# Optimization experiments

Measured on AMD Instinct MI355X. Metric: run time of the kernel, lower is better.

The kernel has to match this reference:

```python
import jax, jax.numpy as jnp
import numpy as np
from jax import lax

EQN = 10  # equations per pixel in FlowLayer


def build_a(h, w):
    """Dense constraint basis a[num, EQN, 4*num] (<=2 nonzeros per row), as in FlowLayer.__init__."""
    num = h * w
    a = np.zeros((num, EQN, 4 * num), np.float32)
    for i in range(num):
        right = (i + 1) % w != 0 and i + 1 < num
        down = i + w < num
        if right:
            a[i, 0, 2 * num + i] = 1.0; a[i, 0, i + 1] = -1.0
            a[i, 2, 2 * num + i] = 1.0; a[i, 2, 2 * num + i + 1] = -1.0
            a[i, 4, i] = 1.0;           a[i, 4, i + 1] = -1.0
            a[i, 6, 3 * num + i] = 1.0; a[i, 6, 3 * num + i + 1] = -1.0
            a[i, 8, num + i] = 1.0;     a[i, 8, num + i + 1] = -1.0
        if down:
            a[i, 1, 3 * num + i] = 1.0; a[i, 1, num + i + w] = -1.0
            a[i, 3, 3 * num + i] = 1.0; a[i, 3, 3 * num + i + w] = -1.0
            a[i, 5, num + i] = 1.0;     a[i, 5, num + i + w] = -1.0
            a[i, 7, 2 * num + i] = 1.0; a[i, 7, 2 * num + i + w] = -1.0
            a[i, 9, i] = 1.0;           a[i, 9, i + w] = -1.0
    last = num - 1  # anchor equations for the last pixel
    a[last, 0, 2 * num + last] = 1.0
    a[last, 1, 3 * num + last] = 1.0
    a[last, 2, 2 * num + last] = 1.0
    a[last, 3, 3 * num + last] = 1.0
    a[last, 4, last] = 1.0
    a[last, 5, num + last] = 1.0
    a[last, 6, 3 * num + last] = 1.0
    a[last, 7, 2 * num + last] = 1.0
    a[last, 8, num + last] = 1.0
    a[last, 9, last] = 1.0
    return a


def conv2d(x, w, b):
    y = lax.conv_general_dilated(x, w, (1, 1), 'SAME',
                                 dimension_numbers=('NCHW', 'OIHW', 'NCHW'))
    return y + b[None, :, None, None]


def setup_inputs() -> dict:
    key = jax.random.key(0)
    N, C, H, W, GR = 4, 64, 16, 16, 4
    ks = jax.random.split(key, 12)
    s3, s1 = 0.04, 0.1  # ~1/sqrt(fan_in) scales
    inp = {
        'x': jax.random.normal(ks[0], (N, C, H, W), jnp.float32),
        'grad_w1': jax.random.normal(ks[1], (C, C, 3, 3), jnp.float32) * s3,
        'grad_b1': jnp.zeros((C,), jnp.float32),
        'grad_w2': jax.random.normal(ks[2], (EQN * GR, C, 3, 3), jnp.float32) * s3,
        'grad_b2': jnp.zeros((EQN * GR,), jnp.float32),
        'att_w1': jax.random.normal(ks[3], (C, C, 3, 3), jnp.float32) * s3,
        'att_b1': jnp.zeros((C,), jnp.float32),
        'att_w2': jax.random.normal(ks[4], (EQN * GR, C, 3, 3), jnp.float32) * s3,
        'att_b2': jnp.zeros((EQN * GR,), jnp.float32),
        'se_w1': jax.random.normal(ks[5], (C // 2, C, 1, 1), jnp.float32) * s1,
        'se_b1': jnp.zeros((C // 2,), jnp.float32),
        'se_w2': jax.random.normal(ks[6], (4 * GR, C // 2, 1, 1), jnp.float32) * s1,
        'se_b2': jnp.zeros((4 * GR,), jnp.float32),
        'gn_w': jnp.ones((4 * GR,), jnp.float32),
        'gn_b': jnp.zeros((4 * GR,), jnp.float32),
        'post_w': jax.random.normal(ks[7], (128, 4 * GR, 3, 3), jnp.float32) * s1,
        'post_b': jnp.zeros((128,), jnp.float32),
    }
    return inp


def reference(x, grad_w1, grad_b1, grad_w2, grad_b2,
              att_w1, att_b1, att_w2, att_b2,
              se_w1, se_b1, se_w2, se_b2,
              gn_w, gn_b, post_w, post_b):
    n, c, h, w = x.shape
    gr = gn_w.shape[0] // 4
    num = h * w
    lrelu = lambda t: jax.nn.leaky_relu(t, 0.01)

    grad = conv2d(lrelu(conv2d(x, grad_w1, grad_b1)), grad_w2, grad_b2)      # [n, eqn*gr, h, w]
    att = jax.nn.sigmoid(conv2d(lrelu(conv2d(x, att_w1, att_b1)), att_w2, att_b2))
    pooled = x.mean((2, 3), keepdims=True)                                     # AdaptiveAvgPool2d(1)
    se = jax.nn.sigmoid(conv2d(lrelu(conv2d(pooled, se_w1, se_b1)), se_w2, se_b2))  # [n, 4*gr, 1, 1]

    # reshape(n*gr, EQN, hw).permute -> [B, hw, EQN] -> flatten rows as (pixel, eqn)
    att_f = att.reshape(n * gr, EQN, num).transpose(0, 2, 1).reshape(n * gr, num * EQN)
    grad_f = grad.reshape(n * gr, EQN, num).transpose(0, 2, 1).reshape(n * gr, num * EQN)

    a_flat = jnp.asarray(build_a(h, w)).reshape(num * EQN, 4 * num)  # constant basis
    A = att_f[:, :, None] * a_flat[None]                 # [B, num*EQN, 4*num]
    b_vec = att_f * grad_f                               # [B, num*EQN]
    ATA = jnp.einsum('brj,brk->bjk', A, A)               # [B, 4num, 4num]
    ATB = jnp.einsum('brj,br->bj', A, b_vec)[..., None]  # [B, 4num, 1]
    jitter = jnp.eye(4 * num, dtype=x.dtype) * 1e-12
    sol = jnp.linalg.solve(ATA + jitter[None], ATB)      # [B, 4num, 1]

    y = sol.reshape(n, 4 * gr, h, w)
    # GroupNorm(1, 4*gr): normalize over (C,H,W) per sample
    mu = y.mean((1, 2, 3), keepdims=True)
    var = ((y - mu) ** 2).mean((1, 2, 3), keepdims=True)
    y = (y - mu) / jnp.sqrt(var + 1e-5)
    y = y * gn_w[None, :, None, None] + gn_b[None, :, None, None]
    y = se * y
    return conv2d(y, post_w, post_b)  # [n, 128, h, w]
```

## Files before the change

kernel.cpp:

```cpp
#include <hip/hip_runtime.h>

#define NCHEB 8

typedef __attribute__((ext_vector_type(8))) short vs8;
typedef __attribute__((ext_vector_type(4))) float vf4;
typedef __attribute__((ext_vector_type(16))) float vf16;

__device__ __forceinline__ unsigned short f2bf(float f) {
  union { float f; unsigned int u; } x; x.f = f;
  unsigned int r = (x.u + 0x7FFFu + ((x.u >> 16) & 1u)) >> 16;
  return (unsigned short)r;
}

template<int COUT, int TILES, bool SE>
__global__ __launch_bounds__(256) void k_conv(
    const float* __restrict__ inA, const float* __restrict__ inB,
    const float* __restrict__ wA, const float* __restrict__ bA,
    const float* __restrict__ wB, const float* __restrict__ bB,
    float* __restrict__ outA, float* __restrict__ outB,
    int actA, int actB,
    const float* __restrict__ x,
    const float* __restrict__ sw1, const float* __restrict__ sb1,
    const float* __restrict__ sw2, const float* __restrict__ sb2,
    float* __restrict__ seo) {
  __shared__ unsigned short Xl[256 * 64];
  __shared__ unsigned short Wl[9 * 16 * 64];
  __shared__ float sp[64];
  __shared__ float sh1[32];
  const int b = blockIdx.x;
  const int t = threadIdx.x;

  if (SE && b >= 8 * TILES) {
    const int n = b - 8 * TILES;
    const int c = t >> 2, part = t & 3;
    const float* xp = x + (n * 64 + c) * 256 + part * 64;
    float s = 0.f;
    for (int k = 0; k < 64; ++k) s += xp[k];
    s += __shfl_xor(s, 1, 64);
    s += __shfl_xor(s, 2, 64);
    if (part == 0) sp[c] = s * (1.f / 256.f);
    __syncthreads();
    if (t < 32) {
      float a = sb1[t];
      for (int k = 0; k < 64; ++k) a += sw1[t * 64 + k] * sp[k];
      sh1[t] = a > 0.f ? a : 0.01f * a;
    }
    __syncthreads();
    if (t < 16) {
      float a = sb2[t];
      for (int k = 0; k < 32; ++k) a += sw2[t * 32 + k] * sh1[k];
      seo[n * 16 + t] = 1.f / (1.f + __expf(-a));
    }
    return;
  }

  const int n = b & 3;
  const int q = b >> 2;
  const int br = (q >= TILES) ? 1 : 0;
  const int ct = q - br * TILES;
  const int co0 = ct * 16;
  const float* inp = (br ? inB : inA) + n * 64 * 256;
  const float* wsrc = br ? wB : wA;
  const float* bias = br ? bB : bA;
  float* outp = (br ? outB : outA) + n * COUT * 256;
  const int act = br ? actB : actA;

  {
    const int p = t;
    #pragma unroll
    for (int q8 = 0; q8 < 8; ++q8) {
      vs8 v;
      #pragma unroll
      for (int j = 0; j < 8; ++j) v[j] = (short)f2bf(inp[(8 * q8 + j) * 256 + p]);
      *(vs8*)&Xl[p * 64 + ((q8 ^ (p & 7)) << 3)] = v;
    }
  }
  {
    const int col = t >> 4;
    const int sub = t & 15;
    const int co = co0 + col;
    if (co < COUT) {
      const float* wp = wsrc + (co * 64 + sub * 4) * 9;
      #pragma unroll
      for (int cc = 0; cc < 4; ++cc) {
        const int ci = sub * 4 + cc;
        #pragma unroll
        for (int e = 0; e < 9; ++e)
          Wl[(e * 16 + col) * 64 + (ci ^ ((col & 7) << 3))] = f2bf(wp[cc * 9 + e]);
      }
    } else {
      #pragma unroll
      for (int cc = 0; cc < 4; ++cc) {
        const int ci = sub * 4 + cc;
        #pragma unroll
        for (int e = 0; e < 9; ++e)
          Wl[(e * 16 + col) * 64 + (ci ^ ((col & 7) << 3))] = 0;
      }
    }
  }
  __syncthreads();

  const int w = t >> 6, lane = t & 63;
  const int px = lane & 15, kg = lane >> 4;
  vf4 acc[4];
  #pragma unroll
  for (int mt = 0; mt < 4; ++mt) acc[mt] = (vf4)0.f;

  for (int e = 0; e < 9; ++e) {
    const int dy = e / 3 - 1, dx = e % 3 - 1;
    const bool xok = (dx == 0) || (dx < 0 ? (px > 0) : (px < 15));
    const int xoff = xok ? dx : 0;
    #pragma unroll
    for (int ks = 0; ks < 2; ++ks) {
      vs8 bf = *(const vs8*)&Wl[(e * 16 + px) * 64 + (((ks * 4 + kg) ^ (px & 7)) << 3)];
      #pragma unroll
      for (int mt = 0; mt < 4; ++mt) {
        const int yy = 4 * w + mt + dy;
        if (yy < 0 || yy > 15) continue;
        const int ps = yy * 16 + px + xoff;
        vs8 a = *(const vs8*)&Xl[ps * 64 + (((ks * 4 + kg) ^ (ps & 7)) << 3)];
        if (!xok) a = (vs8)(short)0;
        acc[mt] = __builtin_amdgcn_mfma_f32_16x16x32_bf16(a, bf, acc[mt], 0, 0, 0);
      }
    }
  }

  const int co = co0 + px;
  if (co < COUT) {
    const float bv = bias[co];
    #pragma unroll
    for (int mt = 0; mt < 4; ++mt) {
      const int y = 4 * w + mt;
      vf4 v = acc[mt];
      #pragma unroll
      for (int j = 0; j < 4; ++j) {
        float s = v[j] + bv;
        if (act == 1) s = s > 0.f ? s : 0.01f * s;
        else if (act == 2) s = 1.f / (1.f + __expf(-s));
        v[j] = s;
      }
      *(vf4*)&outp[co * 256 + y * 16 + kg * 4] = v;
    }
  }
}

__global__ __launch_bounds__(512) void k_post(
    const float* __restrict__ sol, const float* __restrict__ se,
    const float* __restrict__ gn_w, const float* __restrict__ gn_b,
    const float* __restrict__ pw, const float* __restrict__ pb,
    float* __restrict__ out) {
  __shared__ unsigned short Hl[256 * 24];
  __shared__ unsigned short Wp[9 * 128 * 24];
  __shared__ float rs[8];
  __shared__ float rs2[8];
  const int n = blockIdx.x;
  const int t = threadIdx.x;
  const int w = t >> 6, lane = t & 63;

  float v[8];
  {
    const vf4* s4 = (const vf4*)(sol + n * 4096 + 8 * t);
    vf4 a = s4[0], b = s4[1];
    v[0]=a[0];v[1]=a[1];v[2]=a[2];v[3]=a[3];v[4]=b[0];v[5]=b[1];v[6]=b[2];v[7]=b[3];
  }
  float s = 0.f, s2 = 0.f;
  #pragma unroll
  for (int k = 0; k < 8; ++k) { s += v[k]; s2 += v[k] * v[k]; }
  #pragma unroll
  for (int o = 1; o <= 32; o <<= 1) { s += __shfl_xor(s, o, 64); s2 += __shfl_xor(s2, o, 64); }
  if (lane == 0) { rs[w] = s; rs2[w] = s2; }

  {
    const int co = t >> 2, sub = t & 3;
    const float* wp0 = pw + (co * 16 + sub * 4) * 9;
    #pragma unroll
    for (int cc = 0; cc < 4; ++cc) {
      const int ci = sub * 4 + cc;
      #pragma unroll
      for (int e = 0; e < 9; ++e)
        Wp[(e * 128 + co) * 24 + ci] = f2bf(wp0[cc * 9 + e]);
    }
  }
  __syncthreads();
  float sm = 0.f, sq = 0.f;
  #pragma unroll
  for (int k = 0; k < 8; ++k) { sm += rs[k]; sq += rs2[k]; }
  const float mu = sm * (1.f / 4096.f);
  const float rstd = rsqrtf(sq * (1.f / 4096.f) - mu * mu + 1e-5f);

  const int c = t >> 5;
  const int p0 = (8 * t) & 255;
  const float sev = se[n * 16 + c];
  const float sc = rstd * gn_w[c] * sev;
  const float of = (gn_b[c] - mu * rstd * gn_w[c]) * sev;
  #pragma unroll
  for (int k = 0; k < 8; ++k) Hl[(p0 + k) * 24 + c] = f2bf(v[k] * sc + of);
  __syncthreads();

  const int cl = lane & 31, h = lane >> 5;
  const int px = cl & 15, y0 = 2 * w + (cl >> 4);
  vf16 acc[4];
  #pragma unroll
  for (int nt = 0; nt < 4; ++nt) acc[nt] = (vf16)0.f;
  for (int e = 0; e < 9; ++e) {
    const int dy = e / 3 - 1, dx = e % 3 - 1;
    const int yy = y0 + dy, xx = px + dx;
    const bool ok = (yy >= 0 && yy < 16 && xx >= 0 && xx < 16);
    const int ps = ok ? yy * 16 + xx : 0;
    vs8 a = *(const vs8*)&Hl[ps * 24 + h * 8];
    if (!ok) a = (vs8)(short)0;
    #pragma unroll
    for (int nt = 0; nt < 4; ++nt) {
      vs8 bf = *(const vs8*)&Wp[(e * 128 + nt * 32 + cl) * 24 + h * 8];
      acc[nt] = __builtin_amdgcn_mfma_f32_32x32x16_bf16(a, bf, acc[nt], 0, 0, 0);
    }
  }
  float* op = out + n * 32768;
  #pragma unroll
  for (int nt = 0; nt < 4; ++nt) {
    const int co = nt * 32 + cl;
    const float bv = pb[co];
    #pragma unroll
    for (int rq = 0; rq < 4; ++rq) {
      vf4 vv;
      #pragma unroll
      for (int j = 0; j < 4; ++j) vv[j] = acc[nt][rq * 4 + j] + bv;
      *(vf4*)&op[co * 256 + 32 * w + 8 * rq + 4 * h] = vv;
    }
  }
}

__global__ __launch_bounds__(64) void k_pcg(
    const float* __restrict__ att, const float* __restrict__ grad,
    float* __restrict__ sol, int maxit, float tol2) {
  const int sys = blockIdx.x >> 1;
  const int wv = blockIdx.x & 1;
  const int l = threadIdx.x;
  const int row = l >> 2, c4 = l & 3;
  const int i0 = 4 * l;

  const int n = sys >> 2, g = sys & 3;
  const float* ab = att + (n * 40 + g * 10) * 256;
  const float* gb = grad + (n * 40 + g * 10) * 256;

  int era, eda, erb, edb, ec, fa, fb;
  if (wv == 0) { fa = 0; fb = 2; era = 4; eda = 9; erb = 2; edb = 7; ec = 0; }
  else         { fa = 1; fb = 3; era = 8; eda = 5; erb = 6; edb = 3; ec = 1; }

  auto L4 = [](const float* p) { return *reinterpret_cast<const float4*>(p); };
  auto unp = [](float4 v, float* o) { o[0] = v.x; o[1] = v.y; o[2] = v.z; o[3] = v.w; };

  float wLa[4], wRa[4], wUa[4], wDa[4], wXa[4], dga[4], iva[4], rsa[4];
  float wLb[4], wRb[4], wUb[4], wDb[4], wXb[4], dgb[4], ivb[4], rsb[4];

  float rA[4], gA[4], dA[4], hA[4], uA[4] = {0,0,0,0}, vA[4] = {0,0,0,0};
  unp(L4(ab + era * 256 + i0), rA); unp(L4(gb + era * 256 + i0), gA);
  unp(L4(ab + eda * 256 + i0), dA); unp(L4(gb + eda * 256 + i0), hA);
  if (row > 0) { unp(L4(ab + eda * 256 + i0 - 16), uA); unp(L4(gb + eda * 256 + i0 - 16), vA); }
  float rlA = (l > 0) ? ab[era * 256 + i0 - 1] : 0.f;
  float glA = (l > 0) ? gb[era * 256 + i0 - 1] : 0.f;
  float cX[4], gX[4], cU[4] = {0,0,0,0}, gU[4] = {0,0,0,0};
  unp(L4(ab + ec * 256 + i0), cX); unp(L4(gb + ec * 256 + i0), gX);
  float clX = 0.f, glX = 0.f;
  if (wv == 0) { if (l > 0) { clX = ab[ec * 256 + i0 - 1]; glX = gb[ec * 256 + i0 - 1]; } }
  else if (row > 0) { unp(L4(ab + ec * 256 + i0 - 16), cU); unp(L4(gb + ec * 256 + i0 - 16), gU); }

  #pragma unroll
  for (int k = 0; k < 4; ++k) {
    wRa[k] = (k < 3 || c4 < 3) ? rA[k] * rA[k] : 0.f;
    wLa[k] = (k > 0) ? rA[k-1] * rA[k-1] : ((c4 > 0) ? rlA * rlA : 0.f);
    wDa[k] = (row < 15) ? dA[k] * dA[k] : 0.f;
    wUa[k] = (row > 0) ? uA[k] * uA[k] : 0.f;
    float rhs = wRa[k] * gA[k] - wLa[k] * ((k > 0) ? gA[k-1] : glA)
              + wDa[k] * hA[k] - wUa[k] * vA[k];
    float wx, gx;
    if (wv == 0) {
      wx = (k > 0) ? cX[k-1] * cX[k-1] : ((c4 > 0) ? clX * clX : 0.f);
      gx = (k > 0) ? gX[k-1] : glX;
    } else {
      wx = (row > 0) ? cU[k] * cU[k] : 0.f;
      gx = gU[k];
    }
    wXa[k] = wx;
    rhs -= wx * gx;
    rsa[k] = rhs;
    dga[k] = 1e-12f + wRa[k] + wLa[k] + wDa[k] + wUa[k] + wx;
  }

  float rB[4], gB[4], dB[4], hB[4], uB[4] = {0,0,0,0}, vB[4] = {0,0,0,0};
  unp(L4(ab + erb * 256 + i0), rB); unp(L4(gb + erb * 256 + i0), gB);
  unp(L4(ab + edb * 256 + i0), dB); unp(L4(gb + edb * 256 + i0), hB);
  if (row > 0) { unp(L4(ab + edb * 256 + i0 - 16), uB); unp(L4(gb + edb * 256 + i0 - 16), vB); }
  float rlB = (l > 0) ? ab[erb * 256 + i0 - 1] : 0.f;
  float glB = (l > 0) ? gb[erb * 256 + i0 - 1] : 0.f;

  #pragma unroll
  for (int k = 0; k < 4; ++k) {
    wRb[k] = (k < 3 || c4 < 3) ? rB[k] * rB[k] : 0.f;
    wLb[k] = (k > 0) ? rB[k-1] * rB[k-1] : ((c4 > 0) ? rlB * rlB : 0.f);
    wDb[k] = (row < 15) ? dB[k] * dB[k] : 0.f;
    wUb[k] = (row > 0) ? uB[k] * uB[k] : 0.f;
    float wx;
    if (wv == 0) wx = (k < 3 || c4 < 3) ? cX[k] * cX[k] : 0.f;
    else         wx = (row < 15) ? cX[k] * cX[k] : 0.f;
    wXb[k] = wx;
    rsb[k] = wRb[k] * gB[k] - wLb[k] * ((k > 0) ? gB[k-1] : glB)
           + wDb[k] * hB[k] - wUb[k] * vB[k]
           + wx * gX[k];
    dgb[k] = 1e-12f + wRb[k] + wLb[k] + wDb[k] + wUb[k] + wx;
  }

  if (l == 63) {
    float wr = rA[3] * rA[3], wd = dA[3] * dA[3];
    dga[3] += wr + wd;
    rsa[3] += wr * gA[3] + wd * hA[3];
    float wc = cX[3] * cX[3], wrb = rB[3] * rB[3], wdb = dB[3] * dB[3];
    dgb[3] += wc + wrb + wdb;
    rsb[3] += wc * gX[3] + wrb * gB[3] + wdb * hB[3];
  }
  #pragma unroll
  for (int k = 0; k < 4; ++k) { iva[k] = 1.f / dga[k]; ivb[k] = 1.f / dgb[k]; }

  float ua[4], ub[4], wa[4], wb[4];

  auto spmv = [&](const float (&ia_)[4], const float (&ib_)[4],
                  float (&oa)[4], float (&ob)[4]) {
    float aU[4], aD[4], bU[4], bD[4];
    #pragma unroll
    for (int k = 0; k < 4; ++k) {
      aU[k] = __shfl_up(ia_[k], 4, 64);
      aD[k] = __shfl_down(ia_[k], 4, 64);
      bU[k] = __shfl_up(ib_[k], 4, 64);
      bD[k] = __shfl_down(ib_[k], 4, 64);
    }
    float aL = __shfl_up(ia_[3], 1, 64);
    float aR = __shfl_down(ia_[0], 1, 64);
    float bL = __shfl_up(ib_[3], 1, 64);
    float bR = __shfl_down(ib_[0], 1, 64);
    float uaL[4] = {aL, ia_[0], ia_[1], ia_[2]};
    float uaR[4] = {ia_[1], ia_[2], ia_[3], aR};
    float ubL[4] = {bL, ib_[0], ib_[1], ib_[2]};
    float ubR[4] = {ib_[1], ib_[2], ib_[3], bR};
    #pragma unroll
    for (int k = 0; k < 4; ++k) {
      float cA = (wv == 0) ? ubL[k] : bU[k];
      float cB = (wv == 0) ? uaR[k] : aD[k];
      oa[k] = dga[k] * ia_[k] - wLa[k] * uaL[k] - wRa[k] * uaR[k]
            - wUa[k] * aU[k] - wDa[k] * aD[k] - wXa[k] * cA;
      ob[k] = dgb[k] * ib_[k] - wLb[k] * ubL[k] - wRb[k] * ubR[k]
            - wUb[k] * bU[k] - wDb[k] * bD[k] - wXb[k] * cB;
    }
  };

  constexpr float lo = 0.04f, hi = 2.0f;
  constexpr float th = (hi + lo) * 0.5f, dl = (hi - lo) * 0.5f, s1 = th / dl;

  float xa[4] = {0,0,0,0}, xb[4] = {0,0,0,0};
  float ra_[4], rb_[4], pa[4] = {0,0,0,0}, pb_[4] = {0,0,0,0};
  float sa[4] = {0,0,0,0}, sb[4] = {0,0,0,0};
  #pragma unroll
  for (int k = 0; k < 4; ++k) { ra_[k] = rsa[k]; rb_[k] = rsb[k]; }

  auto cheb = [&]() {
    float da_[4], db_[4], ta[4], tb[4], qa[4], qb[4];
    #pragma unroll
    for (int k = 0; k < 4; ++k) {
      da_[k] = (1.0f / th) * iva[k] * ra_[k];
      db_[k] = (1.0f / th) * ivb[k] * rb_[k];
      ua[k] = da_[k]; ub[k] = db_[k];
    }
    spmv(da_, db_, ta, tb);
    #pragma unroll
    for (int k = 0; k < 4; ++k) {
      wa[k] = ta[k]; wb[k] = tb[k];
      qa[k] = ra_[k] - ta[k]; qb[k] = rb_[k] - tb[k];
    }
    float rho = 1.0f / s1;
    #pragma unroll
    for (int j = 1; j < NCHEB; ++j) {
      float rho2 = 1.0f / (2.0f * s1 - rho);
      float c1 = rho2 * rho, c2 = 2.0f * rho2 / dl;
      #pragma unroll
      for (int k = 0; k < 4; ++k) {
        da_[k] = c1 * da_[k] + c2 * iva[k] * qa[k];
        db_[k] = c1 * db_[k] + c2 * ivb[k] * qb[k];
        ua[k] += da_[k]; ub[k] += db_[k];
      }
      spmv(da_, db_, ta, tb);
      #pragma unroll
      for (int k = 0; k < 4; ++k) {
        wa[k] += ta[k]; wb[k] += tb[k];
        qa[k] -= ta[k]; qb[k] -= tb[k];
      }
      rho = rho2;
    }
  };

  float gamma, delta;
  auto dots = [&]() {
    float gp = 0.f, dp = 0.f;
    #pragma unroll
    for (int k = 0; k < 4; ++k) {
      gp += ra_[k] * ua[k] + rb_[k] * ub[k];
      dp += wa[k] * ua[k] + wb[k] * ub[k];
    }
    #pragma unroll
    for (int o = 1; o <= 32; o <<= 1) {
      gp += __shfl_xor(gp, o, 64);
      dp += __shfl_xor(dp, o, 64);
    }
    gamma = gp; delta = dp;
  };

  cheb();
  dots();
  const float thresh = tol2 * gamma;
  float gamma_old = gamma, alpha_old = 1.f;

  for (int it = 0; it < maxit && gamma > thresh; ++it) {
    float beta = (it == 0) ? 0.f : gamma / gamma_old;
    float alpha = (it == 0) ? gamma / delta
                            : gamma / (delta - beta * gamma / alpha_old);
    #pragma unroll
    for (int k = 0; k < 4; ++k) {
      pa[k] = ua[k] + beta * pa[k];   pb_[k] = ub[k] + beta * pb_[k];
      sa[k] = wa[k] + beta * sa[k];   sb[k] = wb[k] + beta * sb[k];
      xa[k] += alpha * pa[k];         xb[k] += alpha * pb_[k];
      ra_[k] -= alpha * sa[k];        rb_[k] -= alpha * sb[k];
    }
    gamma_old = gamma; alpha_old = alpha;
    cheb();
    dots();
  }

  float4* sol4 = reinterpret_cast<float4*>(sol);
  sol4[sys * 256 + fa * 64 + l] = make_float4(xa[0], xa[1], xa[2], xa[3]);
  sol4[sys * 256 + fb * 64 + l] = make_float4(xb[0], xb[1], xb[2], xb[3]);
}

extern "C" void kernel_launch(void* const* d_in, const int* in_sizes, int n_in,
                              void* d_out, int out_size, void* d_ws, size_t ws_size,
                              hipStream_t stream) {
  const float* x       = (const float*)d_in[0];
  const float* grad_w1 = (const float*)d_in[1];
  const float* grad_b1 = (const float*)d_in[2];
  const float* grad_w2 = (const float*)d_in[3];
  const float* grad_b2 = (const float*)d_in[4];
  const float* att_w1  = (const float*)d_in[5];
  const float* att_b1  = (const float*)d_in[6];
  const float* att_w2  = (const float*)d_in[7];
  const float* att_b2  = (const float*)d_in[8];
  const float* se_w1   = (const float*)d_in[9];
  const float* se_b1   = (const float*)d_in[10];
  const float* se_w2   = (const float*)d_in[11];
  const float* se_b2   = (const float*)d_in[12];
  const float* gn_w    = (const float*)d_in[13];
  const float* gn_b    = (const float*)d_in[14];
  const float* post_w  = (const float*)d_in[15];
  const float* post_b  = (const float*)d_in[16];
  float* out = (float*)d_out;
  float* ws = (float*)d_ws;

  float* t1    = ws;
  float* t2    = ws + 65536;
  float* gradb = ws + 131072;
  float* attb  = ws + 172032;
  float* seb   = ws + 212992;
  float* solb  = ws;

  k_conv<64, 4, true><<<36, 256, 0, stream>>>(
      x, x, grad_w1, grad_b1, att_w1, att_b1, t1, t2, 1, 1,
      x, se_w1, se_b1, se_w2, se_b2, seb);
  k_conv<40, 3, false><<<24, 256, 0, stream>>>(
      t1, t2, grad_w2, grad_b2, att_w2, att_b2, gradb, attb, 0, 2,
      nullptr, nullptr, nullptr, nullptr, nullptr, nullptr);
  k_pcg<<<32, 64, 0, stream>>>(attb, gradb, solb, 300, 1e-8f);
  k_post<<<4, 512, 0, stream>>>(solb, seb, gn_w, gn_b, post_w, post_b, out);
}
```

Baseline: 70.50 us.

## Fuse four kernels into one persistent kernel with grid-wide atomic barriers

Replaces the four separate launches (conv1+SE, conv2, PCG solve, post conv) with a single 36-block kernel whose phases are separated by software grid barriers built on atomic counters. This removes per-launch overhead and the gaps between kernels. In exchange it adds a memset launch, spin-wait barriers, packs four PCG waves per block and halves post-phase threads (256 instead of 512), so that phase does more serial work per block. All blocks must be co-resident for the barriers to avoid deadlock.

```diff
diff --git a/kernel.cpp b/kernel.cpp
--- a/kernel.cpp
+++ b/kernel.cpp
@@ -12,50 +12,26 @@
   return (unsigned short)r;
 }
 
-template<int COUT, int TILES, bool SE>
-__global__ __launch_bounds__(256) void k_conv(
+__device__ __forceinline__ void gbar(unsigned* c, int nblk) {
+  __syncthreads();
+  if (threadIdx.x == 0) {
+    __hip_atomic_fetch_add(c, 1u, __ATOMIC_ACQ_REL, __HIP_MEMORY_SCOPE_AGENT);
+    while (__hip_atomic_load(c, __ATOMIC_ACQUIRE, __HIP_MEMORY_SCOPE_AGENT) < (unsigned)nblk)
+      __builtin_amdgcn_s_sleep(1);
+  }
+  __syncthreads();
+}
+
+template<int COUT, int TILES>
+__device__ __forceinline__ void conv_phase(
+    int q, int n,
     const float* __restrict__ inA, const float* __restrict__ inB,
     const float* __restrict__ wA, const float* __restrict__ bA,
     const float* __restrict__ wB, const float* __restrict__ bB,
     float* __restrict__ outA, float* __restrict__ outB,
     int actA, int actB,
-    const float* __restrict__ x,
-    const float* __restrict__ sw1, const float* __restrict__ sb1,
-    const float* __restrict__ sw2, const float* __restrict__ sb2,
-    float* __restrict__ seo) {
-  __shared__ unsigned short Xl[256 * 64];
-  __shared__ unsigned short Wl[9 * 16 * 64];
-  __shared__ float sp[64];
-  __shared__ float sh1[32];
-  const int b = blockIdx.x;
+    unsigned short* Xl, unsigned short* Wl) {
   const int t = threadIdx.x;
-
-  if (SE && b >= 8 * TILES) {
-    const int n = b - 8 * TILES;
-    const int c = t >> 2, part = t & 3;
-    const float* xp = x + (n * 64 + c) * 256 + part * 64;
-    float s = 0.f;
-    for (int k = 0; k < 64; ++k) s += xp[k];
-    s += __shfl_xor(s, 1, 64);
-    s += __shfl_xor(s, 2, 64);
-    if (part == 0) sp[c] = s * (1.f / 256.f);
-    __syncthreads();
-    if (t < 32) {
-      float a = sb1[t];
-      for (int k = 0; k < 64; ++k) a += sw1[t * 64 + k] * sp[k];
-      sh1[t] = a > 0.f ? a : 0.01f * a;
-    }
-    __syncthreads();
-    if (t < 16) {
-      float a = sb2[t];
-      for (int k = 0; k < 32; ++k) a += sw2[t * 32 + k] * sh1[k];
-      seo[n * 16 + t] = 1.f / (1.f + __expf(-a));
-    }
-    return;
-  }
-
-  const int n = b & 3;
-  const int q = b >> 2;
   const int br = (q >= TILES) ? 1 : 0;
   const int ct = q - br * TILES;
   const int co0 = ct * 16;
@@ -144,98 +120,39 @@
   }
 }
 
-__global__ __launch_bounds__(512) void k_post(
-    const float* __restrict__ sol, const float* __restrict__ se,
-    const float* __restrict__ gn_w, const float* __restrict__ gn_b,
-    const float* __restrict__ pw, const float* __restrict__ pb,
-    float* __restrict__ out) {
-  __shared__ unsigned short Hl[256 * 24];
-  __shared__ unsigned short Wp[9 * 128 * 24];
-  __shared__ float rs[8];
-  __shared__ float rs2[8];
-  const int n = blockIdx.x;
+__device__ __forceinline__ void se_phase(
+    int n, const float* __restrict__ x,
+    const float* __restrict__ sw1, const float* __restrict__ sb1,
+    const float* __restrict__ sw2, const float* __restrict__ sb2,
+    float* __restrict__ seo, float* sp, float* sh1) {
   const int t = threadIdx.x;
-  const int w = t >> 6, lane = t & 63;
-
-  float v[8];
-  {
-    const vf4* s4 = (const vf4*)(sol + n * 4096 + 8 * t);
-    vf4 a = s4[0], b = s4[1];
-    v[0]=a[0];v[1]=a[1];v[2]=a[2];v[3]=a[3];v[4]=b[0];v[5]=b[1];v[6]=b[2];v[7]=b[3];
-  }
-  float s = 0.f, s2 = 0.f;
-  #pragma unroll
-  for (int k = 0; k < 8; ++k) { s += v[k]; s2 += v[k] * v[k]; }
-  #pragma unroll
-  for (int o = 1; o <= 32; o <<= 1) { s += __shfl_xor(s, o, 64); s2 += __shfl_xor(s2, o, 64); }
-  if (lane == 0) { rs[w] = s; rs2[w] = s2; }
-
-  {
-    const int co = t >> 2, sub = t & 3;
-    const float* wp0 = pw + (co * 16 + sub * 4) * 9;
-    #pragma unroll
-    for (int cc = 0; cc < 4; ++cc) {
-      const int ci = sub * 4 + cc;
-      #pragma unroll
-      for (int e = 0; e < 9; ++e)
-        Wp[(e * 128 + co) * 24 + ci] = f2bf(wp0[cc * 9 + e]);
-    }
-  }
-  __syncthreads();
-  float sm = 0.f, sq = 0.f;
-  #pragma unroll
-  for (int k = 0; k < 8; ++k) { sm += rs[k]; sq += rs2[k]; }
-  const float mu = sm * (1.f / 4096.f);
-  const float rstd = rsqrtf(sq * (1.f / 4096.f) - mu * mu + 1e-5f);
-
-  const int c = t >> 5;
-  const int p0 = (8 * t) & 255;
-  const float sev = se[n * 16 + c];
-  const float sc = rstd * gn_w[c] * sev;
-  const float of = (gn_b[c] - mu * rstd * gn_w[c]) * sev;
-  #pragma unroll
-  for (int k = 0; k < 8; ++k) Hl[(p0 + k) * 24 + c] = f2bf(v[k] * sc + of);
-  __syncthreads();
-
-  const int cl = lane & 31, h = lane >> 5;
-  const int px = cl & 15, y0 = 2 * w + (cl >> 4);
-  vf16 acc[4];
-  #pragma unroll
-  for (int nt = 0; nt < 4; ++nt) acc[nt] = (vf16)0.f;
-  for (int e = 0; e < 9; ++e) {
-    const int dy = e / 3 - 1, dx = e % 3 - 1;
-    const int yy = y0 + dy, xx = px + dx;
-    const bool ok = (yy >= 0 && yy < 16 && xx >= 0 && xx < 16);
-    const int ps = ok ? yy * 16 + xx : 0;
-    vs8 a = *(const vs8*)&Hl[ps * 24 + h * 8];
-    if (!ok) a = (vs8)(short)0;
-    #pragma unroll
-    for (int nt = 0; nt < 4; ++nt) {
-      vs8 bf = *(const vs8*)&Wp[(e * 128 + nt * 32 + cl) * 24 + h * 8];
-      acc[nt] = __builtin_amdgcn_mfma_f32_32x32x16_bf16(a, bf, acc[nt], 0, 0, 0);
-    }
-  }
-  float* op = out + n * 32768;
-  #pragma unroll
-  for (int nt = 0; nt < 4; ++nt) {
-    const int co = nt * 32 + cl;
-    const float bv = pb[co];
-    #pragma unroll
-    for (int rq = 0; rq < 4; ++rq) {
-      vf4 vv;
-      #pragma unroll
-      for (int j = 0; j < 4; ++j) vv[j] = acc[nt][rq * 4 + j] + bv;
-      *(vf4*)&op[co * 256 + 32 * w + 8 * rq + 4 * h] = vv;
-    }
-  }
-}
-
-__global__ __launch_bounds__(64) void k_pcg(
-    const float* __restrict__ att, const float* __restrict__ grad,
+  const int c = t >> 2, part = t & 3;
+  const float* xp = x + (n * 64 + c) * 256 + part * 64;
+  float s = 0.f;
+  for (int k = 0; k < 64; ++k) s += xp[k];
+  s += __shfl_xor(s, 1, 64);
+  s += __shfl_xor(s, 2, 64);
+  if (part == 0) sp[c] = s * (1.f / 256.f);
+  __syncthreads();
+  if (t < 32) {
+    float a = sb1[t];
+    for (int k = 0; k < 64; ++k) a += sw1[t * 64 + k] * sp[k];
+    sh1[t] = a > 0.f ? a : 0.01f * a;
+  }
+  __syncthreads();
+  if (t < 16) {
+    float a = sb2[t];
+    for (int k = 0; k < 32; ++k) a += sw2[t * 32 + k] * sh1[k];
+    seo[n * 16 + t] = 1.f / (1.f + __expf(-a));
+  }
+}
+
+__device__ void pcg_unit(
+    int unit, const float* __restrict__ att, const float* __restrict__ grad,
     float* __restrict__ sol, int maxit, float tol2) {
-  const int sys = blockIdx.x >> 1;
-  const int wv = blockIdx.x & 1;
-  const int l = threadIdx.x;
+  const int sys = unit >> 1;
+  const int wv = unit & 1;
+  const int l = threadIdx.x & 63;
   const int row = l >> 2, c4 = l & 3;
   const int i0 = 4 * l;
 
@@ -436,6 +353,141 @@
   float4* sol4 = reinterpret_cast<float4*>(sol);
   sol4[sys * 256 + fa * 64 + l] = make_float4(xa[0], xa[1], xa[2], xa[3]);
   sol4[sys * 256 + fb * 64 + l] = make_float4(xb[0], xb[1], xb[2], xb[3]);
+}
+
+__device__ void post_phase(
+    int n, const float* __restrict__ sol, const float* __restrict__ se,
+    const float* __restrict__ gn_w, const float* __restrict__ gn_b,
+    const float* __restrict__ pw, const float* __restrict__ pb,
+    float* __restrict__ out,
+    unsigned short* Hl, unsigned short* Wp, float* rs, float* rs2) {
+  const int t = threadIdx.x;
+  const int w = t >> 6, lane = t & 63;
+
+  float v[16];
+  {
+    const vf4* s4 = (const vf4*)(sol + n * 4096 + 16 * t);
+    #pragma unroll
+    for (int q = 0; q < 4; ++q) {
+      vf4 a = s4[q];
+      v[4*q] = a[0]; v[4*q+1] = a[1]; v[4*q+2] = a[2]; v[4*q+3] = a[3];
+    }
+  }
+  float s = 0.f, s2 = 0.f;
+  #pragma unroll
+  for (int k = 0; k < 16; ++k) { s += v[k]; s2 += v[k] * v[k]; }
+  #pragma unroll
+  for (int o = 1; o <= 32; o <<= 1) { s += __shfl_xor(s, o, 64); s2 += __shfl_xor(s2, o, 64); }
+  if (lane == 0) { rs[w] = s; rs2[w] = s2; }
+
+  {
+    const int co = t >> 1, sub = t & 1;
+    const float* wp0 = pw + (co * 16 + sub * 8) * 9;
+    #pragma unroll
+    for (int cc = 0; cc < 8; ++cc) {
+      const int ci = sub * 8 + cc;
+      #pragma unroll
+      for (int e = 0; e < 9; ++e)
+        Wp[(e * 128 + co) * 24 + ci] = f2bf(wp0[cc * 9 + e]);
+    }
+  }
+  __syncthreads();
+  float sm = 0.f, sq = 0.f;
+  #pragma unroll
+  for (int k = 0; k < 4; ++k) { sm += rs[k]; sq += rs2[k]; }
+  const float mu = sm * (1.f / 4096.f);
+  const float rstd = rsqrtf(sq * (1.f / 4096.f) - mu * mu + 1e-5f);
+
+  const int c = t >> 4;
+  const int p0 = (t & 15) * 16;
+  const float sev = se[n * 16 + c];
+  const float sc = rstd * gn_w[c] * sev;
+  const float of = (gn_b[c] - mu * rstd * gn_w[c]) * sev;
+  #pragma unroll
+  for (int k = 0; k < 16; ++k) Hl[(p0 + k) * 24 + c] = f2bf(v[k] * sc + of);
+  __syncthreads();
+
+  const int cl = lane & 31, h = lane >> 5;
+  const int px = cl & 15;
+  float* op = out + n * 32768;
+  for (int m = 0; m < 2; ++m) {
+    const int mt = 2 * w + m;
+    const int y0 = 2 * mt + (cl >> 4);
+    vf16 acc[4];
+    #pragma unroll
+    for (int nt = 0; nt < 4; ++nt) acc[nt] = (vf16)0.f;
+    for (int e = 0; e < 9; ++e) {
+      const int dy = e / 3 - 1, dx = e % 3 - 1;
+      const int yy = y0 + dy, xx = px + dx;
+      const bool ok = (yy >= 0 && yy < 16 && xx >= 0 && xx < 16);
+      const int ps = ok ? yy * 16 + xx : 0;
+      vs8 a = *(const vs8*)&Hl[ps * 24 + h * 8];
+      if (!ok) a = (vs8)(short)0;
+      #pragma unroll
+      for (int nt = 0; nt < 4; ++nt) {
+        vs8 bf = *(const vs8*)&Wp[(e * 128 + nt * 32 + cl) * 24 + h * 8];
+        acc[nt] = __builtin_amdgcn_mfma_f32_32x32x16_bf16(a, bf, acc[nt], 0, 0, 0);
+      }
+    }
+    #pragma unroll
+    for (int nt = 0; nt < 4; ++nt) {
+      const int co = nt * 32 + cl;
+      const float bv = pb[co];
+      #pragma unroll
+      for (int rq = 0; rq < 4; ++rq) {
+        vf4 vv;
+        #pragma unroll
+        for (int j = 0; j < 4; ++j) vv[j] = acc[nt][rq * 4 + j] + bv;
+        *(vf4*)&op[co * 256 + 32 * mt + 8 * rq + 4 * h] = vv;
+      }
+    }
+  }
+}
+
+__global__ __launch_bounds__(256, 1) void k_fused(
+    const float* __restrict__ x,
+    const float* __restrict__ gw1, const float* __restrict__ gb1,
+    const float* __restrict__ gw2, const float* __restrict__ gb2,
+    const float* __restrict__ aw1, const float* __restrict__ ab1,
+    const float* __restrict__ aw2, const float* __restrict__ ab2,
+    const float* __restrict__ sw1, const float* __restrict__ sb1,
+    const float* __restrict__ sw2, const float* __restrict__ sb2,
+    const float* __restrict__ gnw, const float* __restrict__ gnb,
+    const float* __restrict__ pw, const float* __restrict__ pb,
+    float* __restrict__ t1, float* __restrict__ t2,
+    float* __restrict__ gradb, float* __restrict__ attb,
+    float* __restrict__ seb, float* __restrict__ solb,
+    float* __restrict__ out, unsigned* __restrict__ bar) {
+  __shared__ __attribute__((aligned(16))) unsigned char smem[67648];
+  unsigned short* Xl = (unsigned short*)smem;
+  unsigned short* Wl = (unsigned short*)(smem + 32768);
+  float* sp  = (float*)(smem + 51200);
+  float* sh1 = (float*)(smem + 51456);
+  unsigned short* Hl = (unsigned short*)smem;
+  unsigned short* Wp = (unsigned short*)(smem + 12288);
+  float* rs  = (float*)(smem + 67584);
+  float* rs2 = (float*)(smem + 67616);
+
+  const int bid = blockIdx.x;
+
+  if (bid < 32)
+    conv_phase<64, 4>(bid >> 2, bid & 3, x, x, gw1, gb1, aw1, ab1,
+                      t1, t2, 1, 1, Xl, Wl);
+  else
+    se_phase(bid - 32, x, sw1, sb1, sw2, sb2, seb, sp, sh1);
+  gbar(bar + 0, 36);
+
+  if (bid < 24)
+    conv_phase<40, 3>(bid >> 2, bid & 3, t1, t2, gw2, gb2, aw2, ab2,
+                      gradb, attb, 0, 2, Xl, Wl);
+  gbar(bar + 1, 36);
+
+  if (bid < 8)
+    pcg_unit(bid * 4 + (threadIdx.x >> 6), attb, gradb, solb, 300, 1e-8f);
+  gbar(bar + 2, 36);
+
+  if (bid < 4)
+    post_phase(bid, solb, seb, gnw, gnb, pw, pb, out, Hl, Wp, rs, rs2);
 }
 
 extern "C" void kernel_launch(void* const* d_in, const int* in_sizes, int n_in,
@@ -466,14 +518,14 @@
   float* gradb = ws + 131072;
   float* attb  = ws + 172032;
   float* seb   = ws + 212992;
-  float* solb  = ws;
-
-  k_conv<64, 4, true><<<36, 256, 0, stream>>>(
-      x, x, grad_w1, grad_b1, att_w1, att_b1, t1, t2, 1, 1,
-      x, se_w1, se_b1, se_w2, se_b2, seb);
-  k_conv<40, 3, false><<<24, 256, 0, stream>>>(
-      t1, t2, grad_w2, grad_b2, att_w2, att_b2, gradb, attb, 0, 2,
-      nullptr, nullptr, nullptr, nullptr, nullptr, nullptr);
-  k_pcg<<<32, 64, 0, stream>>>(attb, gradb, solb, 300, 1e-8f);
-  k_post<<<4, 512, 0, stream>>>(solb, seb, gn_w, gn_b, post_w, post_b, out);
-}
+  float* solb  = ws + 213056;
+  unsigned* bar = (unsigned*)(ws + 250000);
+
+  hipMemsetAsync(bar, 0, 16, stream);
+  k_fused<<<36, 256, 0, stream>>>(
+      x, grad_w1, grad_b1, grad_w2, grad_b2,
+      att_w1, att_b1, att_w2, att_b2,
+      se_w1, se_b1, se_w2, se_b2,
+      gn_w, gn_b, post_w, post_b,
+      t1, t2, gradb, attb, seb, solb, out, bar);
+}
```

New measurement: 95.03 us. 1.35x slower.
